# Kernel tuning notes

Hardware: AMD Instinct MI355X
Metric: run time of the kernel (lower is better)

Reference implementation:

```python
import jax, jax.numpy as jnp
import numpy as np

HIDDEN = 1024
HEADS = 16
HEAD_DIM = HIDDEN // HEADS


def setup_inputs() -> dict:
    key = jax.random.key(0)
    ks = jax.random.split(key, 9)
    B, S = 2, 2048
    std = 1.0 / np.sqrt(HIDDEN)
    def lin(k):
        return jax.random.uniform(k, (HIDDEN, HIDDEN), jnp.float32, -std, std)
    def bias(k):
        return jax.random.uniform(k, (HIDDEN,), jnp.float32, -std, std)
    return {
        "x": jax.random.normal(ks[0], (B, S, HIDDEN), jnp.float32),
        "Wq": lin(ks[1]), "bq": bias(ks[2]),
        "Wk": lin(ks[3]), "bk": bias(ks[4]),
        "Wv": lin(ks[5]), "bv": bias(ks[6]),
        "Wo": lin(ks[7]), "bo": bias(ks[8]),
    }


def reference(x, Wq, bq, Wk, bk, Wv, bv, Wo, bo):
    B, S, _ = x.shape
    scale = HEAD_DIM ** -0.5
    # projections; weights stored as (in, out) so y = x @ W + b
    def split_heads(y):
        return y.reshape(B, S, HEADS, HEAD_DIM).transpose(0, 2, 1, 3)  # b h s d
    q = split_heads(x @ Wq + bq)
    k = split_heads(x @ Wk + bk)
    v = split_heads(x @ Wv + bv)
    # dense attention: full [B,H,S,S] score matrix, as in the original
    scores = jnp.einsum("bhsd,bhtd->bhst", q, k) * scale
    attn = jax.nn.softmax(scores, axis=-1)
    out = jnp.einsum("bhst,bhtd->bhsd", attn, v)
    out = out.transpose(0, 2, 1, 3).reshape(B, S, HIDDEN)
    return out @ Wo + bo
```

## Files before the change

kernel.cpp:

```cpp
#include <hip/hip_runtime.h>
#include <hip/hip_bf16.h>

typedef unsigned short u16;
typedef __bf16 bf16x8 __attribute__((ext_vector_type(8)));
typedef float f32x4 __attribute__((ext_vector_type(4)));
typedef float f32x16 __attribute__((ext_vector_type(16)));
typedef unsigned u32x2 __attribute__((ext_vector_type(2)));
typedef unsigned u32x4 __attribute__((ext_vector_type(4)));

#define HIDDEN 1024
#define NH 16
#define HD 64
#define BATCH 2
#define SEQ 2048
#define MTOT (BATCH*SEQ)
#define CEXP 0.18033688f

#if __has_builtin(__builtin_amdgcn_exp2f)
#define EXP2(x) __builtin_amdgcn_exp2f(x)
#else
#define EXP2(x) __builtin_exp2f(x)
#endif

__device__ __forceinline__ u16 f2bf(float f) {
  union { float f; unsigned u; } v; v.f = f;
  unsigned u = v.u;
  return (u16)((u + 0x7fffu + ((u >> 16) & 1u)) >> 16);
}

__device__ __forceinline__ unsigned pack2bf(float a, float b) {
  __hip_bfloat162 h = __float22bfloat162_rn(make_float2(a, b));
  unsigned u; __builtin_memcpy(&u, &h, 4); return u;
}

__device__ __forceinline__ void gload16(const u16* g, u16* l) {
  __builtin_amdgcn_global_load_lds((const __attribute__((address_space(1))) unsigned int*)g,
                                   (__attribute__((address_space(3))) unsigned int*)l, 16, 0, 0);
}

__global__ __launch_bounds__(256) void convert_x_kernel(const float* __restrict__ x,
                                                        u16* __restrict__ xb) {
  size_t i = ((size_t)blockIdx.x * 256 + threadIdx.x) * 4;
  float4 v = *(const float4*)(x + i);
  uint2 p;
  p.x = pack2bf(v.x, v.y);
  p.y = pack2bf(v.z, v.w);
  *(uint2*)(xb + i) = p;
}

__global__ __launch_bounds__(256) void transpose_w_kernel(const float* __restrict__ w0, const float* __restrict__ w1,
                                                          const float* __restrict__ w2, const float* __restrict__ w3,
                                                          u16* __restrict__ dqkv, u16* __restrict__ dwo) {
  __shared__ float t[32][33];
  int z = blockIdx.z;
  const float* src = (z==0) ? w0 : (z==1) ? w1 : (z==2) ? w2 : w3;
  u16* dst = (z < 3) ? (dqkv + (size_t)z * HIDDEN * HIDDEN) : dwo;
  int kb = blockIdx.x * 32, nb = blockIdx.y * 32;
  int tx = threadIdx.x & 31, ty = threadIdx.x >> 5;
  for (int r = ty; r < 32; r += 8) t[r][tx] = src[(size_t)(kb + r) * HIDDEN + nb + tx];
  __syncthreads();
  for (int r = ty; r < 32; r += 8) dst[(size_t)(nb + r) * HIDDEN + kb + tx] = f2bf(t[tx][r]);
}

template<int MODE, int MT>
__global__ __launch_bounds__(256) void gemm_bt(const u16* __restrict__ A, const u16* __restrict__ Bt,
                                               const float* __restrict__ b0, const float* __restrict__ b1,
                                               const float* __restrict__ b2,
                                               u16* __restrict__ Cq, u16* __restrict__ Cv,
                                               float* __restrict__ Cf,
                                               int M, int N, int K) {
  constexpr int MF = MT / 32;
  __shared__ u16 As[2][MT*32];
  __shared__ u16 Bs[2][128*32];
  const int tid = threadIdx.x, lane = tid & 63, wv = tid >> 6;
  const int m0 = blockIdx.x * MT, n0 = blockIdx.y * 128;
  const int wm = (wv >> 1) * (MT/2), wn = (wv & 1) * 64;
  const int col = lane & 15, quad = lane >> 4;
  const int lr = lane >> 2, lk = (lane & 3) * 8;

  auto stage = [&](int kk0, int b) {
    if constexpr (MT == 128) {
      gload16(&A[(size_t)(m0 + wv*32      + lr)*K + kk0 + lk], &As[b][wv*1024]);
      gload16(&A[(size_t)(m0 + wv*32 + 16 + lr)*K + kk0 + lk], &As[b][wv*1024 + 512]);
    } else {
      gload16(&A[(size_t)(m0 + wv*16      + lr)*K + kk0 + lk], &As[b][wv*512]);
    }
    gload16(&Bt[(size_t)(n0 + wv*32      + lr)*K + kk0 + lk], &Bs[b][wv*1024]);
    gload16(&Bt[(size_t)(n0 + wv*32 + 16 + lr)*K + kk0 + lk], &Bs[b][wv*1024 + 512]);
  };

  f32x4 acc[MF][4] = {};
  stage(0, 0);
  __syncthreads();
  int buf = 0;
  for (int k0 = 0; k0 < K; k0 += 32) {
    if (k0 + 32 < K) stage(k0 + 32, buf ^ 1);
    bf16x8 af[MF], bfr[4];
    #pragma unroll
    for (int i = 0; i < MF; i++) af[i]  = *(const bf16x8*)&As[buf][(wm + i*16 + col)*32 + quad*8];
    #pragma unroll
    for (int i = 0; i < 4; i++)  bfr[i] = *(const bf16x8*)&Bs[buf][(wn + i*16 + col)*32 + quad*8];
    #pragma unroll
    for (int mi = 0; mi < MF; mi++)
      #pragma unroll
      for (int ni = 0; ni < 4; ni++)
        acc[mi][ni] = __builtin_amdgcn_mfma_f32_16x16x32_bf16(af[mi], bfr[ni], acc[mi][ni], 0, 0, 0);
    __syncthreads();
    buf ^= 1;
  }
  if constexpr (MODE == 0) {
    #pragma unroll
    for (int mi = 0; mi < MF; mi++)
      #pragma unroll
      for (int ni = 0; ni < 4; ni++) {
        int n = n0 + wn + ni*16 + col;
        float bias = b0[n];
        #pragma unroll
        for (int r = 0; r < 4; r++) {
          int m = m0 + wm + mi*16 + quad*4 + r;
          Cf[(size_t)m*N + n] = acc[mi][ni][r] + bias;
        }
      }
  } else {
    const int seg = n0 >> 10;
    if (seg < 2) {
      const float* bias = (seg == 0) ? b0 : b1;
      const float scl = (seg == 0) ? CEXP : 1.0f;
      #pragma unroll
      for (int mi = 0; mi < MF; mi++)
        #pragma unroll
        for (int ni = 0; ni < 4; ni++) {
          int n = n0 + wn + ni*16 + col;
          float bv = bias[n & (HIDDEN-1)];
          #pragma unroll
          for (int r = 0; r < 4; r++) {
            int m = m0 + wm + mi*16 + quad*4 + r;
            Cq[(size_t)m*N + n] = f2bf((acc[mi][ni][r] + bv) * scl);
          }
        }
    } else {
      const int bb = m0 >> 11;
      #pragma unroll
      for (int mi = 0; mi < MF; mi++)
        #pragma unroll
        for (int ni = 0; ni < 4; ni++) {
          int local = (n0 + wn + ni*16 + col) & (HIDDEN-1);
          int hh = local >> 6, dd = local & 63;
          float bv = b2[local];
          int t4 = (m0 + wm + mi*16 + quad*4) & (SEQ-1);
          uint2 w2;
          w2.x = pack2bf(acc[mi][ni][0] + bv, acc[mi][ni][1] + bv);
          w2.y = pack2bf(acc[mi][ni][2] + bv, acc[mi][ni][3] + bv);
          *(uint2*)&Cv[((size_t)((bb*NH + hh)*HD + dd))*SEQ + t4] = w2;
        }
    }
  }
}

__global__ __launch_bounds__(512, 4) void attn_kernel(const u16* __restrict__ qkv,
                                                      const u16* __restrict__ vt,
                                                      u16* __restrict__ ao) {
  __shared__ u16 SH[19456];
  const int tid = threadIdx.x, lane = tid & 63, wv = tid >> 6;
  const int qt = blockIdx.x, bh = blockIdx.y;
  const int b = bh >> 4, h = bh & 15;
  const int l31 = lane & 31, hl = lane >> 5;
  const int qw = wv & 3, half = wv >> 2;
  const int ht = tid & 255;

  u16* KsH = SH + half*4608;
  u16* VsH = SH + 9216 + half*5120;

  bf16x8 qf[4];
  {
    const u16* qrow = qkv + (size_t)(b*SEQ + qt*128 + qw*32 + l31)*(3*HIDDEN) + h*HD + hl*8;
    #pragma unroll
    for (int kk = 0; kk < 4; kk++) qf[kk] = *(const bf16x8*)(qrow + kk*16);
  }

  f32x16 o[2] = {};
  float rs0 = 0.f, rs1 = 0.f;

  const int rK = ht >> 3, koK = (ht & 7) * 8;
  const int rV = ht >> 2, koV = (ht & 3) * 8;
  const u16* gK = qkv + (size_t)b*SEQ*(3*HIDDEN) + HIDDEN + (size_t)h*HD;
  const u16* gV = vt + (size_t)bh*HD*SEQ;
  const int tb0 = half * 1024;
  uint4 pK = *(const uint4*)&gK[(size_t)(tb0 + rK)*(3*HIDDEN) + koK];
  uint4 pV = *(const uint4*)&gV[(size_t)rV*SEQ + tb0 + koV];

  for (int it = 0; it < 32; ++it) {
    const int curK = (it & 1) * 2304;
    const int curV = (it & 1) * 2560;
    *(uint4*)&KsH[curK + rK*72 + koK] = pK;
    *(uint4*)&VsH[curV + rV*40 + koV] = pV;
    __syncthreads();
    if (it < 31) {
      int tb = tb0 + (it + 1) * 32;
      pK = *(const uint4*)&gK[(size_t)(tb + rK)*(3*HIDDEN) + koK];
      pV = *(const uint4*)&gV[(size_t)rV*SEQ + tb + koV];
    }

    f32x16 s = {};
    __builtin_amdgcn_s_setprio(1);
    #pragma unroll
    for (int kk = 0; kk < 4; kk++) {
      bf16x8 kf = *(const bf16x8*)&KsH[curK + l31*72 + kk*16 + hl*8];
      s = __builtin_amdgcn_mfma_f32_32x32x16_bf16(kf, qf[kk], s, 0, 0, 0);
    }
    __builtin_amdgcn_s_setprio(0);

    unsigned w[8];
    #pragma unroll
    for (int j = 0; j < 8; j++) {
      float p0 = EXP2(s[2*j]);
      float p1 = EXP2(s[2*j+1]);
      rs0 += p0; rs1 += p1;
      w[j] = pack2bf(p0, p1);
    }
    u32x2 r02 = __builtin_amdgcn_permlane32_swap(w[0], w[2], false, false);
    u32x2 r13 = __builtin_amdgcn_permlane32_swap(w[1], w[3], false, false);
    u32x2 r46 = __builtin_amdgcn_permlane32_swap(w[4], w[6], false, false);
    u32x2 r57 = __builtin_amdgcn_permlane32_swap(w[5], w[7], false, false);
    u32x4 c0, c1;
    c0.x = r02[0]; c0.y = r13[0]; c0.z = r02[1]; c0.w = r13[1];
    c1.x = r46[0]; c1.y = r57[0]; c1.z = r46[1]; c1.w = r57[1];
    bf16x8 pf0 = __builtin_bit_cast(bf16x8, c0);
    bf16x8 pf1 = __builtin_bit_cast(bf16x8, c1);

    __builtin_amdgcn_s_setprio(1);
    #pragma unroll
    for (int mt = 0; mt < 2; mt++) {
      bf16x8 vf0 = *(const bf16x8*)&VsH[curV + (mt*32 + l31)*40 + hl*8];
      bf16x8 vf1 = *(const bf16x8*)&VsH[curV + (mt*32 + l31)*40 + 16 + hl*8];
      o[mt] = __builtin_amdgcn_mfma_f32_32x32x16_bf16(vf0, pf0, o[mt], 0, 0, 0);
      o[mt] = __builtin_amdgcn_mfma_f32_32x32x16_bf16(vf1, pf1, o[mt], 0, 0, 0);
    }
    __builtin_amdgcn_s_setprio(0);
  }

  float my = rs0 + rs1;
  float fullh = my + __shfl_xor(my, 32, 64);

  __syncthreads();
  float* cb = (float*)SH;
  if (wv >= 4) {
    const int u = wv - 4;
    #pragma unroll
    for (int mt = 0; mt < 2; mt++)
      #pragma unroll
      for (int r = 0; r < 16; r++)
        cb[u*2048 + (mt*16 + r)*64 + lane] = o[mt][r];
    if (hl == 0) cb[8192 + u*32 + l31] = fullh;
  }
  __syncthreads();
  if (wv < 4) {
    #pragma unroll
    for (int mt = 0; mt < 2; mt++)
      #pragma unroll
      for (int r = 0; r < 16; r++)
        o[mt][r] += cb[wv*2048 + (mt*16 + r)*64 + lane];
    float inv = 1.0f / (fullh + cb[8192 + wv*32 + l31]);

    u16* aop = ao + (size_t)(b*SEQ + qt*128 + wv*32 + l31)*HIDDEN + h*HD + hl*4;
    #pragma unroll
    for (int mt = 0; mt < 2; mt++)
      #pragma unroll
      for (int a4 = 0; a4 < 4; a4++) {
        uint2 w2;
        w2.x = pack2bf(o[mt][4*a4+0]*inv, o[mt][4*a4+1]*inv);
        w2.y = pack2bf(o[mt][4*a4+2]*inv, o[mt][4*a4+3]*inv);
        *(uint2*)&aop[mt*32 + 8*a4] = w2;
      }
  }
}

extern "C" void kernel_launch(void* const* d_in, const int* in_sizes, int n_in,
                              void* d_out, int out_size, void* d_ws, size_t ws_size,
                              hipStream_t stream) {
  const float* x  = (const float*)d_in[0];
  const float* Wq = (const float*)d_in[1];
  const float* bq = (const float*)d_in[2];
  const float* Wk = (const float*)d_in[3];
  const float* bk = (const float*)d_in[4];
  const float* Wv = (const float*)d_in[5];
  const float* bv = (const float*)d_in[6];
  const float* Wo = (const float*)d_in[7];
  const float* bo = (const float*)d_in[8];
  float* out = (float*)d_out;

  char* w = (char*)d_ws;
  u16* xb    = (u16*)w; w += (size_t)MTOT*HIDDEN*2;
  u16* wtqkv = (u16*)w; w += (size_t)3*HIDDEN*HIDDEN*2;
  u16* wto   = (u16*)w; w += (size_t)HIDDEN*HIDDEN*2;
  u16* qkvb  = (u16*)w; w += (size_t)MTOT*3*HIDDEN*2;
  u16* vtb   = (u16*)w; w += (size_t)BATCH*NH*HD*SEQ*2;
  u16* aob   = (u16*)w; w += (size_t)MTOT*HIDDEN*2;

  convert_x_kernel<<<(MTOT*HIDDEN)/1024, 256, 0, stream>>>(x, xb);
  transpose_w_kernel<<<dim3(32, 32, 4), 256, 0, stream>>>(Wq, Wk, Wv, Wo, wtqkv, wto);
  gemm_bt<1,128><<<dim3(32, 24), 256, 0, stream>>>(xb, wtqkv, bq, bk, bv, qkvb, vtb, nullptr, MTOT, 3*HIDDEN, HIDDEN);
  attn_kernel<<<dim3(SEQ/128, BATCH*NH), 512, 0, stream>>>(qkvb, vtb, aob);
  gemm_bt<0,64><<<dim3(64, 8), 256, 0, stream>>>(aob, wto, bo, nullptr, nullptr, nullptr, nullptr, out, MTOT, HIDDEN, HIDDEN);
}
```

Baseline: 133.1 us.

## Triple-buffer GEMM LDS staging with partial vmcnt waits and swizzle workgroup order

Converts the GEMM's double-buffered shared-memory pipeline to three buffers with two tiles in flight. It replaces __syncthreads with explicit s_waitcnt vmcnt waits that only drain the oldest tile's loads before the barrier. It also remaps block indices in a strided swizzle so neighbouring workgroups share A/B tiles in cache. This costs more LDS per block, which may reduce occupancy. The hand-counted vmcnt values must match the number of gload16 issues per stage, or the kernel will race.

```diff
diff --git a/kernel.cpp b/kernel.cpp
--- a/kernel.cpp
+++ b/kernel.cpp
@@ -70,10 +70,13 @@
                                                float* __restrict__ Cf,
                                                int M, int N, int K) {
   constexpr int MF = MT / 32;
-  __shared__ u16 As[2][MT*32];
-  __shared__ u16 Bs[2][128*32];
+  __shared__ u16 As[3][MT*32];
+  __shared__ u16 Bs[3][128*32];
   const int tid = threadIdx.x, lane = tid & 63, wv = tid >> 6;
-  const int m0 = blockIdx.x * MT, n0 = blockIdx.y * 128;
+  const int nwg = gridDim.x * gridDim.y;
+  const int flat = blockIdx.y * gridDim.x + blockIdx.x;
+  const int swz = (flat & 7) * (nwg >> 3) + (flat >> 3);
+  const int m0 = (swz % gridDim.x) * MT, n0 = (swz / gridDim.x) * 128;
   const int wm = (wv >> 1) * (MT/2), wn = (wv & 1) * 64;
   const int col = lane & 15, quad = lane >> 4;
   const int lr = lane >> 2, lk = (lane & 3) * 8;
@@ -88,13 +91,23 @@
     gload16(&Bt[(size_t)(n0 + wv*32      + lr)*K + kk0 + lk], &Bs[b][wv*1024]);
     gload16(&Bt[(size_t)(n0 + wv*32 + 16 + lr)*K + kk0 + lk], &Bs[b][wv*1024 + 512]);
   };
+  auto wait_steady = [&]() {
+    if constexpr (MT == 128) asm volatile("s_waitcnt vmcnt(4)" ::: "memory");
+    else                     asm volatile("s_waitcnt vmcnt(3)" ::: "memory");
+  };
 
   f32x4 acc[MF][4] = {};
+  const int nt = K / 32;
   stage(0, 0);
-  __syncthreads();
-  int buf = 0;
-  for (int k0 = 0; k0 < K; k0 += 32) {
-    if (k0 + 32 < K) stage(k0 + 32, buf ^ 1);
+  stage(32, 1);
+  wait_steady();
+  __builtin_amdgcn_sched_barrier(0);
+  __builtin_amdgcn_s_barrier();
+  __builtin_amdgcn_sched_barrier(0);
+
+  for (int it = 0; it < nt; ++it) {
+    if (it + 2 < nt) stage((it + 2) * 32, (it + 2) % 3);
+    const int buf = it % 3;
     bf16x8 af[MF], bfr[4];
     #pragma unroll
     for (int i = 0; i < MF; i++) af[i]  = *(const bf16x8*)&As[buf][(wm + i*16 + col)*32 + quad*8];
@@ -105,8 +118,13 @@
       #pragma unroll
       for (int ni = 0; ni < 4; ni++)
         acc[mi][ni] = __builtin_amdgcn_mfma_f32_16x16x32_bf16(af[mi], bfr[ni], acc[mi][ni], 0, 0, 0);
-    __syncthreads();
-    buf ^= 1;
+    if (it + 1 < nt) {
+      if (it + 2 < nt) wait_steady();
+      else asm volatile("s_waitcnt vmcnt(0)" ::: "memory");
+      __builtin_amdgcn_sched_barrier(0);
+      __builtin_amdgcn_s_barrier();
+      __builtin_amdgcn_sched_barrier(0);
+    }
   }
   if constexpr (MODE == 0) {
     #pragma unroll
```

Result: slower. 141.1 us (+6.1%).
